# Kernel optimization log

Measured on AMD Instinct MI355X. Metric: run time of the kernel, lower is better.

## Reference

```python
import jax, jax.numpy as jnp
import numpy as np

NEG_SLOPE = 0.2  # PyG GATConv default

def gat_layer(x, src, dst, W, a_src, a_dst, b, N):
    # h = W x  (PyG applies linear before attention)
    h = x @ W                                   # [N, hid]
    al_src = h @ a_src                          # [N]
    al_dst = h @ a_dst                          # [N]
    e = jax.nn.leaky_relu(al_src[src] + al_dst[dst], NEG_SLOPE)  # [E]
    # segment softmax over incoming edges of each destination node
    m = jax.ops.segment_max(e, dst, num_segments=N)
    e = jnp.exp(e - m[dst])
    s = jax.ops.segment_sum(e, dst, num_segments=N)
    coef = e / s[dst]                           # [E]
    out = jax.ops.segment_sum(h[src] * coef[:, None], dst, num_segments=N)
    return out + b

def setup_inputs() -> dict:
    key = jax.random.key(0)
    ks = jax.random.split(key, 12)
    N, E, in_dim, hid, out_dim, G = 100000, 1600000, 128, 64, 1, 256
    x = jax.random.normal(ks[0], (N, in_dim), dtype=jnp.float32)
    edge_index = jax.random.randint(ks[1], (2, E), 0, N, dtype=jnp.int64)
    batch = jnp.sort(jax.random.randint(ks[2], (N,), 0, G, dtype=jnp.int64))
    def glorot(k, shape):
        lim = float(np.sqrt(6.0 / (shape[0] + shape[-1])))
        return jax.random.uniform(k, shape, jnp.float32, -lim, lim)
    return {
        "x": x, "edge_index": edge_index, "batch": batch,
        "W1": glorot(ks[3], (in_dim, hid)),
        "a_src1": glorot(ks[4], (hid,)), "a_dst1": glorot(ks[5], (hid,)),
        "b1": jnp.zeros((hid,), jnp.float32),
        "W2": glorot(ks[6], (hid, hid)),
        "a_src2": glorot(ks[7], (hid,)), "a_dst2": glorot(ks[8], (hid,)),
        "b2": jnp.zeros((hid,), jnp.float32),
        "Wfc": glorot(ks[9], (hid, out_dim)),
        "bfc": jnp.zeros((out_dim,), jnp.float32),
    }

def reference(x, edge_index, batch, W1, a_src1, a_dst1, b1, W2, a_src2, a_dst2, b2, Wfc, bfc):
    N = x.shape[0]
    G = 256  # number of graphs in the batch
    # add self-loops (PyG GATConv default add_self_loops=True)
    loops = jnp.arange(N, dtype=edge_index.dtype)
    src = jnp.concatenate([edge_index[0], loops])
    dst = jnp.concatenate([edge_index[1], loops])
    h = jax.nn.elu(gat_layer(x, src, dst, W1, a_src1, a_dst1, b1, N))
    h = jax.nn.elu(gat_layer(h, src, dst, W2, a_src2, a_dst2, b2, N))
    # global mean pool over graph ids
    sums = jax.ops.segment_sum(h, batch, num_segments=G)
    cnts = jax.ops.segment_sum(jnp.ones((N,), h.dtype), batch, num_segments=G)
    pooled = sums / jnp.maximum(cnts, 1.0)[:, None]
    return pooled @ Wfc + bfc
```

## Files before the change

### kernel.cpp

```cpp
#include <hip/hip_runtime.h>
#include <hip/hip_bf16.h>
#include <cstdint>


#define BIN_SHIFT 7
#define BIN_NODES 128
#define BIN_CAP 3584
#define PLACE_CHUNK 2048

typedef __attribute__((ext_vector_type(8))) short bf16x8;
typedef __attribute__((ext_vector_type(4))) float f32x4;

__device__ __forceinline__ float wave_reduce_sum(float v) {
#pragma unroll
  for (int off = 32; off > 0; off >>= 1) v += __shfl_xor(v, off, 64);
  return v;
}

__device__ __forceinline__ unsigned short f2bf(float f) {
  unsigned int u = __float_as_uint(f);
  u += 0x7fffu + ((u >> 16) & 1u);
  return (unsigned short)(u >> 16);
}
__device__ __forceinline__ float bf2f(unsigned short u) {
  return __uint_as_float(((unsigned int)u) << 16);
}


__global__ __launch_bounds__(256) void setup_kernel(
    const float* __restrict__ W1, unsigned short* __restrict__ w1thi,
    unsigned short* __restrict__ w1tlo, const float* __restrict__ W2,
    unsigned short* __restrict__ w2thi, unsigned short* __restrict__ w2tlo,
    const int* __restrict__ batch, int* __restrict__ gstart,
    int* __restrict__ binCursor, float* __restrict__ pool, int N, int G, int NB) {
  const int b = blockIdx.x;
  const int t = threadIdx.x;
  if (b < 32) {
    int idx = b * 256 + t;
    int n = idx & 63, k = idx >> 6;
    float v = W1[(size_t)k * 64 + n];
    unsigned short h = f2bf(v);
    w1thi[(size_t)n * 128 + k] = h;
    w1tlo[(size_t)n * 128 + k] = f2bf(v - bf2f(h));
  } else if (b < 48) {
    int idx = (b - 32) * 256 + t;
    int n = idx & 63, k = idx >> 6;
    float v = W2[(size_t)k * 64 + n];
    unsigned short h = f2bf(v);
    w2thi[(size_t)n * 64 + k] = h;
    w2tlo[(size_t)n * 64 + k] = f2bf(v - bf2f(h));
  } else if (b < 50) {
    int g = (b - 48) * 256 + t;
    if (g <= G) {
      int lo = 0, hi = N;
      while (lo < hi) {
        int mid = (lo + hi) >> 1;
        if (batch[mid] < g) lo = mid + 1;
        else hi = mid;
      }
      gstart[g] = lo;
    }
  } else if (b < 54) {
    int i = (b - 50) * 256 + t;
    if (i < NB) binCursor[i] = 0;
  } else {
    int i = (b - 54) * 256 + t;
    pool[i] = 0.f;
  }
}


__global__ __launch_bounds__(256) void bin_place_kernel(
    const int* __restrict__ ei, int E, int M, int NB,
    int* __restrict__ binCursor, unsigned int* __restrict__ binned) {
  __shared__ int cur[1024];
  __shared__ int res[1024];
  const int t = threadIdx.x;
  const int cbase = blockIdx.x * PLACE_CHUNK;

  for (int i = t; i < NB; i += 256) cur[i] = 0;
  __syncthreads();

  unsigned int pk[PLACE_CHUNK / 256];
  int br[PLACE_CHUNK / 256];
#pragma unroll
  for (int j = 0; j < PLACE_CHUNK / 256; ++j) {
    int i = cbase + t + j * 256;
    if (i < M) {
      int s, d;
      if (i < E) { s = ei[i]; d = ei[E + i]; } else { s = d = i - E; }
      int b = d >> BIN_SHIFT;
      int r = atomicAdd(&cur[b], 1);
      pk[j] = ((unsigned int)(d & (BIN_NODES - 1)) << 24) | (unsigned int)s;
      br[j] = (b << 16) | r;
    } else {
      br[j] = -1;
    }
  }
  __syncthreads();
  for (int i = t; i < NB; i += 256) {
    int c = cur[i];
    res[i] = c ? atomicAdd(&binCursor[i], c) : 0;
  }
  __syncthreads();
#pragma unroll
  for (int j = 0; j < PLACE_CHUNK / 256; ++j) {
    if (br[j] >= 0) {
      int b = br[j] >> 16;
      int pos = res[b] + (br[j] & 0xFFFF);
      if (pos < BIN_CAP) binned[(size_t)b * BIN_CAP + pos] = pk[j];
    }
  }
}

__global__ __launch_bounds__(512) void csr_finalize_kernel(
    const unsigned int* __restrict__ binned, const int* __restrict__ binCursor,
    int* __restrict__ rowbeg, int* __restrict__ rowend, int* __restrict__ csrc,
    int N, int NB) {
  __shared__ int cnt[128];
  __shared__ int wsum[2];
  const int b = blockIdx.x;
  const int t = threadIdx.x;
  const int nodeBase = b << BIN_SHIFT;
  const int eBase = b * BIN_CAP;
  const int cntE = binCursor[b];

  if (t < 128) cnt[t] = 0;
  __syncthreads();
  for (int i = t; i < cntE; i += 512) {
    atomicAdd(&cnt[binned[eBase + i] >> 24], 1);
  }
  __syncthreads();
  const int lane = t & 63, wv = t >> 6;
  int v = (t < 128) ? cnt[t] : 0;
  int x = v;
#pragma unroll
  for (int o = 1; o < 64; o <<= 1) {
    int u = __shfl_up(x, o, 64);
    if (lane >= o) x += u;
  }
  if (t < 128 && lane == 63) wsum[wv] = x;
  __syncthreads();
  if (t < 128) {
    const int o = ((wv == 1) ? wsum[0] : 0) + x - v;
    int node = nodeBase + t;
    if (node < N) {
      rowbeg[node] = eBase + o;
      rowend[node] = eBase + o + v;
    }
    cnt[t] = o;
  }
  __syncthreads();
  for (int i = t; i < cntE; i += 512) {
    unsigned int pk = binned[eBase + i];
    int r = atomicAdd(&cnt[pk >> 24], 1);
    csrc[eBase + r] = (int)(pk & 0xFFFFFFu);
  }
}


template <int KDIM>
__global__ __launch_bounds__(256) void gemm_mfma(
    const float* __restrict__ A, const unsigned short* __restrict__ Wt_hi,
    const unsigned short* __restrict__ Wt_lo, unsigned short* __restrict__ hb,
    const float* __restrict__ a_src, const float* __restrict__ a_dst,
    float* __restrict__ alsrc, float* __restrict__ aldst, int N) {
  __shared__ unsigned short Ah[64][40], Al[64][40], Bh[64][40], Bl[64][40];
  const int block_m = blockIdx.x * 64;
  const int t = threadIdx.x;
  const int lane = t & 63;
  const int m0 = (t >> 6) * 16;
  const int lc = lane & 15;
  const int lr = lane >> 4;
  const int srow = t >> 2;
  const int skslot = (t & 3) * 8;

  f32x4 acc[4] = {};

  for (int kc = 0; kc < KDIM; kc += 32) {
    {
      int gn = block_m + srow;
      if (gn >= N) gn = N - 1;
      const float4 v0 = *(const float4*)(A + (size_t)gn * KDIM + kc + skslot);
      const float4 v1 = *(const float4*)(A + (size_t)gn * KDIM + kc + skslot + 4);
      float v[8] = {v0.x, v0.y, v0.z, v0.w, v1.x, v1.y, v1.z, v1.w};
      unsigned short h8[8], l8[8];
#pragma unroll
      for (int j = 0; j < 8; ++j) {
        h8[j] = f2bf(v[j]);
        l8[j] = f2bf(v[j] - bf2f(h8[j]));
      }
      *(uint4*)&Ah[srow][skslot] = *(const uint4*)h8;
      *(uint4*)&Al[srow][skslot] = *(const uint4*)l8;
    }
    {
      const uint4 wh = *(const uint4*)(Wt_hi + (size_t)srow * KDIM + kc + skslot);
      const uint4 wl = *(const uint4*)(Wt_lo + (size_t)srow * KDIM + kc + skslot);
      *(uint4*)&Bh[srow][skslot] = wh;
      *(uint4*)&Bl[srow][skslot] = wl;
    }
    __syncthreads();

    const bf16x8 ah = *(const bf16x8*)&Ah[m0 + lc][lr * 8];
    const bf16x8 al = *(const bf16x8*)&Al[m0 + lc][lr * 8];
#pragma unroll
    for (int nf = 0; nf < 4; ++nf) {
      const bf16x8 bh = *(const bf16x8*)&Bh[nf * 16 + lc][lr * 8];
      const bf16x8 bl = *(const bf16x8*)&Bl[nf * 16 + lc][lr * 8];
      acc[nf] = __builtin_amdgcn_mfma_f32_16x16x32_bf16(ah, bh, acc[nf], 0, 0, 0);
      acc[nf] = __builtin_amdgcn_mfma_f32_16x16x32_bf16(ah, bl, acc[nf], 0, 0, 0);
      acc[nf] = __builtin_amdgcn_mfma_f32_16x16x32_bf16(al, bh, acc[nf], 0, 0, 0);
    }
    __syncthreads();
  }

  float as4[4], ad4[4];
#pragma unroll
  for (int nf = 0; nf < 4; ++nf) {
    as4[nf] = a_src[nf * 16 + lc];
    ad4[nf] = a_dst[nf * 16 + lc];
  }
#pragma unroll
  for (int r = 0; r < 4; ++r) {
    const int gn = block_m + m0 + lr * 4 + r;
    float ps = 0.f, pd = 0.f;
#pragma unroll
    for (int nf = 0; nf < 4; ++nf) {
      const float v = acc[nf][r];
      if (gn < N) hb[(size_t)gn * 64 + nf * 16 + lc] = f2bf(v);
      ps += v * as4[nf];
      pd += v * ad4[nf];
    }
#pragma unroll
    for (int off = 1; off < 16; off <<= 1) {
      ps += __shfl_xor(ps, off, 64);
      pd += __shfl_xor(pd, off, 64);
    }
    if (lc == 0 && gn < N) {
      alsrc[gn] = ps;
      aldst[gn] = pd;
    }
  }
}

template <int ELU>
__global__ __launch_bounds__(256) void spmm_fused_kernel(
    const int* __restrict__ rowbeg, const int* __restrict__ rowend,
    const int* __restrict__ csrc,
    const float* __restrict__ alsrc, const float* __restrict__ aldst,
    const unsigned short* __restrict__ hb, const float* __restrict__ bias,
    float* __restrict__ outbuf, int N) {
  const int t = threadIdx.x;
  const int l = t & 15;
  const int gb = t & 48;
  const int half = l >> 3;
  const int f0 = (l & 7) * 8;
  const int node = blockIdx.x * 16 + (t >> 4);
  if (node >= N) return;
  const int start = rowbeg[node];
  const int end = rowend[node];
  const float ad = aldst[node];

  float ssum = 0.f;
  float acc[8] = {};

  int i0 = start + l;
  bool v0 = i0 < end;
  int s = v0 ? csrc[i0] : 0;
  float w;
  {
    float e = alsrc[s] + ad;
    e = (e > 0.f) ? e : 0.2f * e;
    w = v0 ? __expf(fminf(e, 80.f)) : 0.f;
  }

  for (int base = start; base < end; base += 16) {
    int in = base + 16 + l;
    bool vn = in < end;
    int sn = vn ? csrc[in] : 0;
    float aln = alsrc[sn];

    uint4 u[8];
#pragma unroll
    for (int j = 0; j < 8; ++j) {
      int sj = __shfl(s, gb + 2 * j + half, 64);
      u[j] = *(const uint4*)(hb + (size_t)sj * 64 + f0);
    }

    ssum += w;
#pragma unroll
    for (int j = 0; j < 8; ++j) {
      float wj = __shfl(w, gb + 2 * j + half, 64);
      acc[0] += wj * __uint_as_float(u[j].x << 16);
      acc[1] += wj * __uint_as_float(u[j].x & 0xFFFF0000u);
      acc[2] += wj * __uint_as_float(u[j].y << 16);
      acc[3] += wj * __uint_as_float(u[j].y & 0xFFFF0000u);
      acc[4] += wj * __uint_as_float(u[j].z << 16);
      acc[5] += wj * __uint_as_float(u[j].z & 0xFFFF0000u);
      acc[6] += wj * __uint_as_float(u[j].w << 16);
      acc[7] += wj * __uint_as_float(u[j].w & 0xFFFF0000u);
    }

    float en = aln + ad;
    en = (en > 0.f) ? en : 0.2f * en;
    w = vn ? __expf(fminf(en, 80.f)) : 0.f;
    s = sn;
  }

#pragma unroll
  for (int k = 0; k < 8; ++k) acc[k] += __shfl_xor(acc[k], 8, 64);
#pragma unroll
  for (int off = 1; off < 16; off <<= 1) ssum += __shfl_xor(ssum, off, 64);

  if (half == 0) {
    float inv = 1.0f / ssum;
    float r[8];
#pragma unroll
    for (int k = 0; k < 8; ++k) r[k] = acc[k] * inv;
    if (ELU) {
      const float4 b40 = *(const float4*)(bias + f0);
      const float4 b41 = *(const float4*)(bias + f0 + 4);
      r[0] += b40.x; r[1] += b40.y; r[2] += b40.z; r[3] += b40.w;
      r[4] += b41.x; r[5] += b41.y; r[6] += b41.z; r[7] += b41.w;
#pragma unroll
      for (int k = 0; k < 8; ++k) r[k] = (r[k] > 0.f) ? r[k] : expm1f(r[k]);
    }
    *(float4*)(outbuf + (size_t)node * 64 + f0) = make_float4(r[0], r[1], r[2], r[3]);
    *(float4*)(outbuf + (size_t)node * 64 + f0 + 4) = make_float4(r[4], r[5], r[6], r[7]);
  }
}

__global__ __launch_bounds__(256) void post_pool_kernel(
    const float* __restrict__ acc, const float* __restrict__ bias,
    const int* __restrict__ batch, float* __restrict__ pool, int N) {
  __shared__ float4 red4[16][17];
  __shared__ int sB[16];
  __shared__ int uni;
  const int t = threadIdx.x;
  const int ln = t >> 4;
  const int f4 = t & 15;
  const int base = blockIdx.x * 16;
  const int node = base + ln;

  if (t < 16) {
    int nn = base + t;
    sB[t] = (nn < N) ? batch[nn] : -1;
  }
  __syncthreads();
  if (t == 0) {
    int u = (base + 15 < N);
    for (int i = 1; i < 16; i++) u &= (sB[i] == sB[0]);
    uni = u;
  }

  float4 v = make_float4(0.f, 0.f, 0.f, 0.f);
  if (node < N) {
    v = *(const float4*)(acc + ((size_t)node * 16 + f4) * 4);
    const float4 b4 = *(const float4*)(bias + f4 * 4);
    v.x += b4.x; v.y += b4.y; v.z += b4.z; v.w += b4.w;
    v.x = (v.x > 0.f) ? v.x : expm1f(v.x);
    v.y = (v.y > 0.f) ? v.y : expm1f(v.y);
    v.z = (v.z > 0.f) ? v.z : expm1f(v.z);
    v.w = (v.w > 0.f) ? v.w : expm1f(v.w);
  }
  red4[ln][f4] = v;
  __syncthreads();

  if (t < 64) {
    const float* rf = (const float*)red4;
    if (uni) {
      float s = 0.f;
#pragma unroll
      for (int n = 0; n < 16; n++) s += rf[n * 68 + t];
      atomicAdd(&pool[(size_t)sB[0] * 64 + t], s);
    } else {
      for (int n = 0; n < 16; n++) {
        int g = sB[n];
        if (g >= 0) atomicAdd(&pool[(size_t)g * 64 + t], rf[n * 68 + t]);
      }
    }
  }
}

__global__ void final_kernel(const float* __restrict__ pool, const int* __restrict__ gstart,
                             const float* __restrict__ Wfc, const float* __restrict__ bfc,
                             float* __restrict__ out, int G) {
  int wid = (blockIdx.x * blockDim.x + threadIdx.x) >> 6;
  int lane = threadIdx.x & 63;
  if (wid >= G) return;
  float c = (float)max(gstart[wid + 1] - gstart[wid], 1);
  float v = pool[(size_t)wid * 64 + lane] * (1.0f / c) * Wfc[lane];
  v = wave_reduce_sum(v);
  if (lane == 0) out[wid] = v + bfc[0];
}


extern "C" void kernel_launch(void* const* d_in, const int* in_sizes, int n_in,
                              void* d_out, int out_size, void* d_ws, size_t ws_size,
                              hipStream_t stream) {
  const float* x     = (const float*)d_in[0];
  const int*   ei    = (const int*)d_in[1];
  const int*   batch = (const int*)d_in[2];
  const float* W1    = (const float*)d_in[3];
  const float* asrc1 = (const float*)d_in[4];
  const float* adst1 = (const float*)d_in[5];
  const float* b1    = (const float*)d_in[6];
  const float* W2    = (const float*)d_in[7];
  const float* asrc2 = (const float*)d_in[8];
  const float* adst2 = (const float*)d_in[9];
  const float* b2    = (const float*)d_in[10];
  const float* Wfc   = (const float*)d_in[11];
  const float* bfc   = (const float*)d_in[12];
  float* out = (float*)d_out;

  const int N = in_sizes[0] / 128;
  const int E = in_sizes[1] / 2;
  const int G = 256;
  const int M = E + N;
  const int NB = (N + BIN_NODES - 1) >> BIN_SHIFT;

  char* p = (char*)d_ws;
  auto alloc = [&](size_t bytes) {
    char* r = p;
    p += (bytes + 255) & ~size_t(255);
    return r;
  };
  float*          h1e    = (float*)alloc((size_t)N * 64 * 4);
  float*          accbuf = (float*)alloc((size_t)N * 64 * 4);
  unsigned short* hb     = (unsigned short*)alloc((size_t)N * 64 * 2);
  float* alsrc  = (float*)alloc((size_t)N * 4);
  float* aldst  = (float*)alloc((size_t)N * 4);
  int*   rowbeg = (int*)alloc((size_t)N * 4);
  int*   rowend = (int*)alloc((size_t)N * 4);
  int*   csrc   = (int*)alloc((size_t)NB * BIN_CAP * 4);
  unsigned int* binned = (unsigned int*)alloc((size_t)NB * BIN_CAP * 4);
  int*   binCursor = (int*)alloc((size_t)NB * 4);
  float* pool   = (float*)alloc((size_t)G * 64 * 4);
  int*   gstart = (int*)alloc((size_t)(G + 1) * 4);
  unsigned short* w1thi = (unsigned short*)alloc((size_t)64 * 128 * 2);
  unsigned short* w1tlo = (unsigned short*)alloc((size_t)64 * 128 * 2);
  unsigned short* w2thi = (unsigned short*)alloc((size_t)64 * 64 * 2);
  unsigned short* w2tlo = (unsigned short*)alloc((size_t)64 * 64 * 2);

  setup_kernel<<<118, 256, 0, stream>>>(W1, w1thi, w1tlo, W2, w2thi, w2tlo,
                                        batch, gstart, binCursor, pool, N, G, NB);
  bin_place_kernel<<<(M + PLACE_CHUNK - 1) / PLACE_CHUNK, 256, 0, stream>>>(
      ei, E, M, NB, binCursor, binned);
  csr_finalize_kernel<<<NB, 512, 0, stream>>>(binned, binCursor, rowbeg, rowend,
                                              csrc, N, NB);

  gemm_mfma<128><<<(N + 63) / 64, 256, 0, stream>>>(x, w1thi, w1tlo, hb, asrc1, adst1,
                                                    alsrc, aldst, N);
  spmm_fused_kernel<1><<<(N + 15) / 16, 256, 0, stream>>>(rowbeg, rowend, csrc, alsrc,
                                                          aldst, hb, b1, h1e, N);

  gemm_mfma<64><<<(N + 63) / 64, 256, 0, stream>>>(h1e, w2thi, w2tlo, hb, asrc2, adst2,
                                                   alsrc, aldst, N);
  spmm_fused_kernel<0><<<(N + 15) / 16, 256, 0, stream>>>(rowbeg, rowend, csrc, alsrc,
                                                          aldst, hb, nullptr, accbuf, N);
  post_pool_kernel<<<(N + 15) / 16, 256, 0, stream>>>(accbuf, b2, batch, pool, N);

  final_kernel<<<(G * 64 + 255) / 256, 256, 0, stream>>>(pool, gstart, Wfc, bfc, out, G);
}
```

Before: 269.6 us.

## Merge setup with edge binning and CSR finalize with first GEMM

Merges the setup work (weight split, graph start search, pool zeroing) and the edge bin-placement into a single launch that branches on block index. It also runs the per-bin CSR finalize and the layer-1 MFMA GEMM as independent block groups in one kernel. The bin cursor reset moves to a memset, and finalize now uses 256 threads instead of 512. The goal is fewer kernel launches and letting independent work overlap. The risk is a race: placement blocks read w1thi/w1tlo only through the GEMM, which now runs in the next launch, so ordering holds, but finalize blocks get half as many threads.

Result: no change. 264.7 us (-1.8%).

```diff
diff --git a/kernel.cpp b/kernel.cpp
--- a/kernel.cpp
+++ b/kernel.cpp
@@ -7,6 +7,7 @@
 #define BIN_NODES 128
 #define BIN_CAP 3584
 #define PLACE_CHUNK 2048
+#define SETUP_BLOCKS 114
 
 typedef __attribute__((ext_vector_type(8))) short bf16x8;
 typedef __attribute__((ext_vector_type(4))) float f32x4;
@@ -26,15 +27,19 @@
   return __uint_as_float(((unsigned int)u) << 16);
 }
 
-
-__global__ __launch_bounds__(256) void setup_kernel(
+__global__ __launch_bounds__(256) void mega_a_kernel(
     const float* __restrict__ W1, unsigned short* __restrict__ w1thi,
     unsigned short* __restrict__ w1tlo, const float* __restrict__ W2,
     unsigned short* __restrict__ w2thi, unsigned short* __restrict__ w2tlo,
     const int* __restrict__ batch, int* __restrict__ gstart,
-    int* __restrict__ binCursor, float* __restrict__ pool, int N, int G, int NB) {
+    float* __restrict__ pool, const int* __restrict__ ei, int E, int M,
+    int NB, int* __restrict__ binCursor, unsigned int* __restrict__ binned,
+    int N, int G) {
+  __shared__ int cur[1024];
+  __shared__ int res[1024];
   const int b = blockIdx.x;
   const int t = threadIdx.x;
+
   if (b < 32) {
     int idx = b * 256 + t;
     int n = idx & 63, k = idx >> 6;
@@ -42,6 +47,7 @@
     unsigned short h = f2bf(v);
     w1thi[(size_t)n * 128 + k] = h;
     w1tlo[(size_t)n * 128 + k] = f2bf(v - bf2f(h));
+    return;
   } else if (b < 48) {
     int idx = (b - 32) * 256 + t;
     int n = idx & 63, k = idx >> 6;
@@ -49,6 +55,7 @@
     unsigned short h = f2bf(v);
     w2thi[(size_t)n * 64 + k] = h;
     w2tlo[(size_t)n * 64 + k] = f2bf(v - bf2f(h));
+    return;
   } else if (b < 50) {
     int g = (b - 48) * 256 + t;
     if (g <= G) {
@@ -60,24 +67,14 @@
       }
       gstart[g] = lo;
     }
-  } else if (b < 54) {
+    return;
+  } else if (b < SETUP_BLOCKS) {
     int i = (b - 50) * 256 + t;
-    if (i < NB) binCursor[i] = 0;
-  } else {
-    int i = (b - 54) * 256 + t;
     pool[i] = 0.f;
-  }
-}
-
-
-__global__ __launch_bounds__(256) void bin_place_kernel(
-    const int* __restrict__ ei, int E, int M, int NB,
-    int* __restrict__ binCursor, unsigned int* __restrict__ binned) {
-  __shared__ int cur[1024];
-  __shared__ int res[1024];
-  const int t = threadIdx.x;
-  const int cbase = blockIdx.x * PLACE_CHUNK;
-
+    return;
+  }
+
+  const int cbase = (b - SETUP_BLOCKS) * PLACE_CHUNK;
   for (int i = t; i < NB; i += 256) cur[i] = 0;
   __syncthreads();
 
@@ -89,10 +86,10 @@
     if (i < M) {
       int s, d;
       if (i < E) { s = ei[i]; d = ei[E + i]; } else { s = d = i - E; }
-      int b = d >> BIN_SHIFT;
-      int r = atomicAdd(&cur[b], 1);
+      int bb = d >> BIN_SHIFT;
+      int r = atomicAdd(&cur[bb], 1);
       pk[j] = ((unsigned int)(d & (BIN_NODES - 1)) << 24) | (unsigned int)s;
-      br[j] = (b << 16) | r;
+      br[j] = (bb << 16) | r;
     } else {
       br[j] = -1;
     }
@@ -106,55 +103,140 @@
 #pragma unroll
   for (int j = 0; j < PLACE_CHUNK / 256; ++j) {
     if (br[j] >= 0) {
-      int b = br[j] >> 16;
-      int pos = res[b] + (br[j] & 0xFFFF);
-      if (pos < BIN_CAP) binned[(size_t)b * BIN_CAP + pos] = pk[j];
-    }
-  }
-}
-
-__global__ __launch_bounds__(512) void csr_finalize_kernel(
+      int bb = br[j] >> 16;
+      int pos = res[bb] + (br[j] & 0xFFFF);
+      if (pos < BIN_CAP) binned[(size_t)bb * BIN_CAP + pos] = pk[j];
+    }
+  }
+}
+
+__global__ __launch_bounds__(256) void finalize_gemm_kernel(
     const unsigned int* __restrict__ binned, const int* __restrict__ binCursor,
     int* __restrict__ rowbeg, int* __restrict__ rowend, int* __restrict__ csrc,
-    int N, int NB) {
-  __shared__ int cnt[128];
-  __shared__ int wsum[2];
-  const int b = blockIdx.x;
+    int NB,
+    const float* __restrict__ A, const unsigned short* __restrict__ Wt_hi,
+    const unsigned short* __restrict__ Wt_lo, unsigned short* __restrict__ hb,
+    const float* __restrict__ a_src, const float* __restrict__ a_dst,
+    float* __restrict__ alsrc, float* __restrict__ aldst, int N) {
+  __shared__ unsigned short Ah[64][40], Al[64][40], Bh[64][40], Bl[64][40];
   const int t = threadIdx.x;
-  const int nodeBase = b << BIN_SHIFT;
-  const int eBase = b * BIN_CAP;
-  const int cntE = binCursor[b];
-
-  if (t < 128) cnt[t] = 0;
-  __syncthreads();
-  for (int i = t; i < cntE; i += 512) {
-    atomicAdd(&cnt[binned[eBase + i] >> 24], 1);
-  }
-  __syncthreads();
-  const int lane = t & 63, wv = t >> 6;
-  int v = (t < 128) ? cnt[t] : 0;
-  int x = v;
-#pragma unroll
-  for (int o = 1; o < 64; o <<= 1) {
-    int u = __shfl_up(x, o, 64);
-    if (lane >= o) x += u;
-  }
-  if (t < 128 && lane == 63) wsum[wv] = x;
-  __syncthreads();
-  if (t < 128) {
-    const int o = ((wv == 1) ? wsum[0] : 0) + x - v;
-    int node = nodeBase + t;
-    if (node < N) {
-      rowbeg[node] = eBase + o;
-      rowend[node] = eBase + o + v;
-    }
-    cnt[t] = o;
-  }
-  __syncthreads();
-  for (int i = t; i < cntE; i += 512) {
-    unsigned int pk = binned[eBase + i];
-    int r = atomicAdd(&cnt[pk >> 24], 1);
-    csrc[eBase + r] = (int)(pk & 0xFFFFFFu);
+
+  if (blockIdx.x < NB) {
+    int* cnt = (int*)&Ah[0][0];
+    int* wsum = (int*)&Bh[0][0];
+    const int b = blockIdx.x;
+    const int nodeBase = b << BIN_SHIFT;
+    const int eBase = b * BIN_CAP;
+    const int cntE = binCursor[b];
+
+    if (t < 128) cnt[t] = 0;
+    __syncthreads();
+    for (int i = t; i < cntE; i += 256) {
+      atomicAdd(&cnt[binned[eBase + i] >> 24], 1);
+    }
+    __syncthreads();
+    const int lane = t & 63, wv = t >> 6;
+    int v = (t < 128) ? cnt[t] : 0;
+    int x = v;
+#pragma unroll
+    for (int o = 1; o < 64; o <<= 1) {
+      int u = __shfl_up(x, o, 64);
+      if (lane >= o) x += u;
+    }
+    if (t < 128 && lane == 63) wsum[wv] = x;
+    __syncthreads();
+    if (t < 128) {
+      const int o = ((wv == 1) ? wsum[0] : 0) + x - v;
+      int node = nodeBase + t;
+      if (node < N) {
+        rowbeg[node] = eBase + o;
+        rowend[node] = eBase + o + v;
+      }
+      cnt[t] = o;
+    }
+    __syncthreads();
+    for (int i = t; i < cntE; i += 256) {
+      unsigned int pk = binned[eBase + i];
+      int r = atomicAdd(&cnt[pk >> 24], 1);
+      csrc[eBase + r] = (int)(pk & 0xFFFFFFu);
+    }
+    return;
+  }
+
+  constexpr int KDIM = 128;
+  const int block_m = (blockIdx.x - NB) * 64;
+  const int lane = t & 63;
+  const int m0 = (t >> 6) * 16;
+  const int lc = lane & 15;
+  const int lr = lane >> 4;
+  const int srow = t >> 2;
+  const int skslot = (t & 3) * 8;
+
+  f32x4 acc[4] = {};
+
+  for (int kc = 0; kc < KDIM; kc += 32) {
+    {
+      int gn = block_m + srow;
+      if (gn >= N) gn = N - 1;
+      const float4 v0 = *(const float4*)(A + (size_t)gn * KDIM + kc + skslot);
+      const float4 v1 = *(const float4*)(A + (size_t)gn * KDIM + kc + skslot + 4);
+      float v[8] = {v0.x, v0.y, v0.z, v0.w, v1.x, v1.y, v1.z, v1.w};
+      unsigned short h8[8], l8[8];
+#pragma unroll
+      for (int j = 0; j < 8; ++j) {
+        h8[j] = f2bf(v[j]);
+        l8[j] = f2bf(v[j] - bf2f(h8[j]));
+      }
+      *(uint4*)&Ah[srow][skslot] = *(const uint4*)h8;
+      *(uint4*)&Al[srow][skslot] = *(const uint4*)l8;
+    }
+    {
+      const uint4 wh = *(const uint4*)(Wt_hi + (size_t)srow * KDIM + kc + skslot);
+      const uint4 wl = *(const uint4*)(Wt_lo + (size_t)srow * KDIM + kc + skslot);
+      *(uint4*)&Bh[srow][skslot] = wh;
+      *(uint4*)&Bl[srow][skslot] = wl;
+    }
+    __syncthreads();
+
+    const bf16x8 ah = *(const bf16x8*)&Ah[m0 + lc][lr * 8];
+    const bf16x8 al = *(const bf16x8*)&Al[m0 + lc][lr * 8];
+#pragma unroll
+    for (int nf = 0; nf < 4; ++nf) {
+      const bf16x8 bh = *(const bf16x8*)&Bh[nf * 16 + lc][lr * 8];
+      const bf16x8 bl = *(const bf16x8*)&Bl[nf * 16 + lc][lr * 8];
+      acc[nf] = __builtin_amdgcn_mfma_f32_16x16x32_bf16(ah, bh, acc[nf], 0, 0, 0);
+      acc[nf] = __builtin_amdgcn_mfma_f32_16x16x32_bf16(ah, bl, acc[nf], 0, 0, 0);
+      acc[nf] = __builtin_amdgcn_mfma_f32_16x16x32_bf16(al, bh, acc[nf], 0, 0, 0);
+    }
+    __syncthreads();
+  }
+
+  float as4[4], ad4[4];
+#pragma unroll
+  for (int nf = 0; nf < 4; ++nf) {
+    as4[nf] = a_src[nf * 16 + lc];
+    ad4[nf] = a_dst[nf * 16 + lc];
+  }
+#pragma unroll
+  for (int r = 0; r < 4; ++r) {
+    const int gn = block_m + m0 + lr * 4 + r;
+    float ps = 0.f, pd = 0.f;
+#pragma unroll
+    for (int nf = 0; nf < 4; ++nf) {
+      const float v = acc[nf][r];
+      if (gn < N) hb[(size_t)gn * 64 + nf * 16 + lc] = f2bf(v);
+      ps += v * as4[nf];
+      pd += v * ad4[nf];
+    }
+#pragma unroll
+    for (int off = 1; off < 16; off <<= 1) {
+      ps += __shfl_xor(ps, off, 64);
+      pd += __shfl_xor(pd, off, 64);
+    }
+    if (lc == 0 && gn < N) {
+      alsrc[gn] = ps;
+      aldst[gn] = pd;
+    }
   }
 }
 
@@ -418,6 +500,7 @@
   const int G = 256;
   const int M = E + N;
   const int NB = (N + BIN_NODES - 1) >> BIN_SHIFT;
+  const int NPLACE = (M + PLACE_CHUNK - 1) / PLACE_CHUNK;
 
   char* p = (char*)d_ws;
   auto alloc = [&](size_t bytes) {
@@ -442,15 +525,15 @@
   unsigned short* w2thi = (unsigned short*)alloc((size_t)64 * 64 * 2);
   unsigned short* w2tlo = (unsigned short*)alloc((size_t)64 * 64 * 2);
 
-  setup_kernel<<<118, 256, 0, stream>>>(W1, w1thi, w1tlo, W2, w2thi, w2tlo,
-                                        batch, gstart, binCursor, pool, N, G, NB);
-  bin_place_kernel<<<(M + PLACE_CHUNK - 1) / PLACE_CHUNK, 256, 0, stream>>>(
-      ei, E, M, NB, binCursor, binned);
-  csr_finalize_kernel<<<NB, 512, 0, stream>>>(binned, binCursor, rowbeg, rowend,
-                                              csrc, N, NB);
-
-  gemm_mfma<128><<<(N + 63) / 64, 256, 0, stream>>>(x, w1thi, w1tlo, hb, asrc1, adst1,
-                                                    alsrc, aldst, N);
+  hipMemsetAsync(binCursor, 0, (size_t)NB * 4, stream);
+  mega_a_kernel<<<SETUP_BLOCKS + NPLACE, 256, 0, stream>>>(
+      W1, w1thi, w1tlo, W2, w2thi, w2tlo, batch, gstart, pool,
+      ei, E, M, NB, binCursor, binned, N, G);
+
+  finalize_gemm_kernel<<<NB + (N + 63) / 64, 256, 0, stream>>>(
+      binned, binCursor, rowbeg, rowend, csrc, NB,
+      x, w1thi, w1tlo, hb, asrc1, adst1, alsrc, aldst, N);
+
   spmm_fused_kernel<1><<<(N + 15) / 16, 256, 0, stream>>>(rowbeg, rowend, csrc, alsrc,
                                                           aldst, hb, b1, h1e, N);
 
```
